# Performance work log

Hardware: AMD Instinct MI355X
Metric: run time of the kernel (lower is better)

The kernel has to match this reference:

```python
import jax, jax.numpy as jnp
import numpy as np

NX, NZ, NU, B = 16, 8, 4, 65536


def setup_inputs() -> dict:
    key = jax.random.key(0)
    ks = jax.random.split(key, 10)
    mu_prev = jax.random.normal(ks[0], (B, NX), dtype=jnp.float32)
    # PSD covariance per batch element: L L^T + 0.5 I
    L = 0.1 * jax.random.normal(ks[1], (B, NX, NX), dtype=jnp.float32)
    Sigma_prev = jnp.einsum('bij,bkj->bik', L, L) + 0.5 * jnp.eye(NX, dtype=jnp.float32)
    u = jax.random.normal(ks[2], (B, NU), dtype=jnp.float32)
    z = jax.random.normal(ks[3], (B, NZ), dtype=jnp.float32)
    # System matrices (shared across the batch); scaled to keep tanh unsaturated
    A = 0.1 * jax.random.normal(ks[4], (NX, NX), dtype=jnp.float32) + jnp.eye(NX, dtype=jnp.float32)
    Bm = 0.1 * jax.random.normal(ks[5], (NX, NU), dtype=jnp.float32)
    C = 0.2 * jax.random.normal(ks[6], (NZ, NX), dtype=jnp.float32)
    MQ = 0.1 * jax.random.normal(ks[7], (NZ, NZ), dtype=jnp.float32)
    Q = MQ @ MQ.T + 0.05 * jnp.eye(NZ, dtype=jnp.float32)   # measurement noise cov [nz,nz]
    MR = 0.1 * jax.random.normal(ks[8], (NX, NX), dtype=jnp.float32)
    R = MR @ MR.T + 0.01 * jnp.eye(NX, dtype=jnp.float32)   # process noise cov [nx,nx]
    return {'mu_prev': mu_prev, 'Sigma_prev': Sigma_prev, 'u': u, 'z': z,
            'A': A, 'Bm': Bm, 'C': C, 'Q': Q, 'R': R}


def reference(mu_prev, Sigma_prev, u, z, A, Bm, C, Q, R):
    # Discrete-time EKF propagate (already_discrete=True branch), batched via vmap.
    def f_sys(x, u):
        return jnp.tanh(A @ x + Bm @ u)

    def h_sys(x):
        return jnp.tanh(C @ x)

    I_nx = jnp.eye(NX, dtype=mu_prev.dtype)

    def step(mu, Sig, u_b, z_b):
        mu_bar = f_sys(mu, u_b)                      # [nx]
        G = jax.jacfwd(f_sys)(mu, u_b)               # [nx,nx] df/dx
        Sig_bar = R + G @ Sig @ G.T                  # [nx,nx]
        H = jax.jacfwd(h_sys)(mu_bar)                # [nz,nx] dh/dx
        tp = Sig_bar @ H.T                           # [nx,nz]
        K = tp @ jnp.linalg.inv(H @ tp + Q)          # [nx,nz] Kalman gain
        mu_now = mu_bar + K @ (z_b - h_sys(mu_bar))
        I_KH = I_nx - K @ H
        Sig_now = I_KH @ Sig_bar @ I_KH.T + K @ Q @ K.T  # Joseph form
        return mu_now, Sig_now

    return jax.vmap(step)(mu_prev, Sigma_prev, u, z)
```

## Files before the change

### kernel.cpp

```cpp
#include <hip/hip_runtime.h>
#include <math.h>


namespace {

constexpr int GROUPS = 16;
constexpr int TPB    = GROUPS * 16;

constexpr int O_VT  = 0;
constexpr int O_TPT = 0;
constexpr int O_SI  = 128;
constexpr int O_PIV = 192;
constexpr int O_VB  = 256;
constexpr int GS    = 312;

__device__ __forceinline__ float dot4(float4 a, float4 b) {
  return a.x*b.x + a.y*b.y + a.z*b.z + a.w*b.w;
}

__device__ __forceinline__ float tanh_fast(float x) {
  float e = __expf(2.0f * x);
  return 1.0f - 2.0f * __builtin_amdgcn_rcpf(e + 1.0f);
}

__global__ __launch_bounds__(TPB)
void ekf_kernel(const float* __restrict__ mu_prev,
                const float* __restrict__ Sig_prev,
                const float* __restrict__ U,
                const float* __restrict__ Z,
                const float* __restrict__ A,
                const float* __restrict__ Bm,
                const float* __restrict__ C,
                const float* __restrict__ Q,
                const float* __restrict__ R,
                float* __restrict__ mu_out,
                float* __restrict__ sig_out,
                int Btot)
{
  __shared__ float lds[GS * GROUPS];
  const int tid = threadIdx.x;
  const int g = tid >> 4;
  const int t = tid & 15;
  int e = blockIdx.x * GROUPS + g;
  if (e >= Btot) e = Btot - 1;
  float* L = lds + g * GS;

  float sig[16];
  {
    const float4* sp = (const float4*)(Sig_prev + (size_t)e * 256 + t * 16);
    #pragma unroll
    for (int c = 0; c < 4; c++) {
      float4 v = sp[c];
      sig[4*c+0] = v.x; sig[4*c+1] = v.y; sig[4*c+2] = v.z; sig[4*c+3] = v.w;
    }
  }

  float pre;
  {
    const float4* ar = (const float4*)(A + t * 16);
    const float4* mr = (const float4*)(mu_prev + (size_t)e * 16);
    pre = dot4(ar[0], mr[0]) + dot4(ar[1], mr[1])
        + dot4(ar[2], mr[2]) + dot4(ar[3], mr[3]);
    float4 b4 = *(const float4*)(Bm + t * 4);
    float4 u4 = *(const float4*)(U + (size_t)e * 4);
    pre += dot4(b4, u4);
  }
  const float mubar = tanh_fast(pre);
  const float dloc  = 1.0f - mubar * mubar;
  L[O_VB + t]      = mubar;
  L[O_VB + 16 + t] = dloc;
  __builtin_amdgcn_wave_barrier();

  if (t < 8) {
    const float4* cr = (const float4*)(C + t * 16);
    const float4* mb = (const float4*)(L + O_VB);
    float ph = dot4(cr[0], mb[0]) + dot4(cr[1], mb[1])
             + dot4(cr[2], mb[2]) + dot4(cr[3], mb[3]);
    float hb = tanh_fast(ph);
    L[O_VB + 32 + t] = hb;
    L[O_VB + 40 + t] = 1.0f - hb * hb;
  }
  __builtin_amdgcn_wave_barrier();

  float dh[8];
  {
    float4 d0 = *(const float4*)(L + O_VB + 40);
    float4 d1 = *(const float4*)(L + O_VB + 44);
    dh[0]=d0.x; dh[1]=d0.y; dh[2]=d0.z; dh[3]=d0.w;
    dh[4]=d1.x; dh[5]=d1.y; dh[6]=d1.z; dh[7]=d1.w;
  }

  #pragma unroll
  for (int j = 0; j < 16; j++) {
    float acc = 0.f;
    #pragma unroll
    for (int k = 0; k < 16; k++) acc += sig[k] * A[j*16 + k];
    L[O_VT + j*16 + t] = acc;
  }
  __builtin_amdgcn_wave_barrier();

  float sb[16];
  {
    float vcol[16];
    const float4* vt = (const float4*)(L + O_VT + t*16);
    #pragma unroll
    for (int c = 0; c < 4; c++) {
      float4 v = vt[c];
      vcol[4*c+0]=v.x; vcol[4*c+1]=v.y; vcol[4*c+2]=v.z; vcol[4*c+3]=v.w;
    }
    #pragma unroll
    for (int i = 0; i < 16; i++) {
      float acc = 0.f;
      #pragma unroll
      for (int k = 0; k < 16; k++) acc += A[i*16 + k] * vcol[k];
      sb[i] = acc;
    }
  }
  __builtin_amdgcn_wave_barrier();

  {
    const float4* rr = (const float4*)(R + t * 16);
    const float4* dv = (const float4*)(L + O_VB + 16);
    #pragma unroll
    for (int c = 0; c < 4; c++) {
      float4 r4 = rr[c];
      float4 d4 = dv[c];
      sb[4*c+0] = r4.x + dloc * sb[4*c+0] * d4.x;
      sb[4*c+1] = r4.y + dloc * sb[4*c+1] * d4.y;
      sb[4*c+2] = r4.z + dloc * sb[4*c+2] * d4.z;
      sb[4*c+3] = r4.w + dloc * sb[4*c+3] * d4.w;
    }
  }

  float tp[8];
  #pragma unroll
  for (int m = 0; m < 8; m++) {
    float acc = 0.f;
    #pragma unroll
    for (int k = 0; k < 16; k++) acc += sb[k] * C[m*16 + k];
    tp[m] = acc * dh[m];
    L[O_TPT + m*16 + t] = tp[m];
  }
  __builtin_amdgcn_wave_barrier();

  if (t < 8) {
    float tcol[16];
    const float4* tt = (const float4*)(L + O_TPT + t*16);
    #pragma unroll
    for (int c = 0; c < 4; c++) {
      float4 v = tt[c];
      tcol[4*c+0]=v.x; tcol[4*c+1]=v.y; tcol[4*c+2]=v.z; tcol[4*c+3]=v.w;
    }
    float s8[8];
    {
      float4 q0 = *(const float4*)(Q + t*8);
      float4 q1 = *(const float4*)(Q + t*8 + 4);
      float qv[8] = {q0.x,q0.y,q0.z,q0.w,q1.x,q1.y,q1.z,q1.w};
      #pragma unroll
      for (int m = 0; m < 8; m++) {
        float acc = 0.f;
        #pragma unroll
        for (int k = 0; k < 16; k++) acc += C[m*16 + k] * tcol[k];
        s8[m] = acc * dh[m] + qv[m];
      }
    }

    float x8[8];
    #pragma unroll
    for (int j = 0; j < 8; j++) x8[j] = (j == t) ? 1.0f : 0.0f;
    #pragma unroll
    for (int p = 0; p < 8; p++) {
      if (t == p) {
        float rcp = 1.0f / s8[p];
        #pragma unroll
        for (int j = 0; j < 8; j++) { s8[j] *= rcp; x8[j] *= rcp; }
        *((float4*)(L + O_PIV + 0))  = make_float4(s8[0], s8[1], s8[2], s8[3]);
        *((float4*)(L + O_PIV + 4))  = make_float4(s8[4], s8[5], s8[6], s8[7]);
        *((float4*)(L + O_PIV + 8))  = make_float4(x8[0], x8[1], x8[2], x8[3]);
        *((float4*)(L + O_PIV + 12)) = make_float4(x8[4], x8[5], x8[6], x8[7]);
      }
      __builtin_amdgcn_wave_barrier();
      if (t != p) {
        float f = s8[p];
        float4 pa = *(const float4*)(L + O_PIV + 0);
        float4 pb = *(const float4*)(L + O_PIV + 4);
        float4 pc = *(const float4*)(L + O_PIV + 8);
        float4 pd = *(const float4*)(L + O_PIV + 12);
        s8[0]-=f*pa.x; s8[1]-=f*pa.y; s8[2]-=f*pa.z; s8[3]-=f*pa.w;
        s8[4]-=f*pb.x; s8[5]-=f*pb.y; s8[6]-=f*pb.z; s8[7]-=f*pb.w;
        x8[0]-=f*pc.x; x8[1]-=f*pc.y; x8[2]-=f*pc.z; x8[3]-=f*pc.w;
        x8[4]-=f*pd.x; x8[5]-=f*pd.y; x8[6]-=f*pd.z; x8[7]-=f*pd.w;
      }
      __builtin_amdgcn_wave_barrier();
    }
    *((float4*)(L + O_SI + t*8 + 0)) = make_float4(x8[0], x8[1], x8[2], x8[3]);
    *((float4*)(L + O_SI + t*8 + 4)) = make_float4(x8[4], x8[5], x8[6], x8[7]);
  }
  __builtin_amdgcn_wave_barrier();

  float kreg[8] = {0,0,0,0,0,0,0,0};
  #pragma unroll
  for (int m = 0; m < 8; m++) {
    float tpm = tp[m];
    float4 a = *(const float4*)(L + O_SI + m*8 + 0);
    float4 b = *(const float4*)(L + O_SI + m*8 + 4);
    kreg[0]+=tpm*a.x; kreg[1]+=tpm*a.y; kreg[2]+=tpm*a.z; kreg[3]+=tpm*a.w;
    kreg[4]+=tpm*b.x; kreg[5]+=tpm*b.y; kreg[6]+=tpm*b.z; kreg[7]+=tpm*b.w;
  }

  {
    float4 z0 = *(const float4*)(Z + (size_t)e * 8);
    float4 z1 = *(const float4*)(Z + (size_t)e * 8 + 4);
    float4 h0 = *(const float4*)(L + O_VB + 32);
    float4 h1 = *(const float4*)(L + O_VB + 36);
    float mu_now = mubar
      + kreg[0]*(z0.x-h0.x) + kreg[1]*(z0.y-h0.y)
      + kreg[2]*(z0.z-h0.z) + kreg[3]*(z0.w-h0.w)
      + kreg[4]*(z1.x-h1.x) + kreg[5]*(z1.y-h1.y)
      + kreg[6]*(z1.z-h1.z) + kreg[7]*(z1.w-h1.w);
    mu_out[(size_t)e * 16 + t] = mu_now;
  }

  float out[16];
  #pragma unroll
  for (int i = 0; i < 16; i++) out[i] = sb[i];
  #pragma unroll
  for (int m = 0; m < 8; m++) {
    const float km = kreg[m];
    const float4* tr = (const float4*)(L + O_TPT + m*16);
    float4 t0 = tr[0], t1 = tr[1], t2 = tr[2], t3 = tr[3];
    out[0]  -= km*t0.x; out[1]  -= km*t0.y; out[2]  -= km*t0.z; out[3]  -= km*t0.w;
    out[4]  -= km*t1.x; out[5]  -= km*t1.y; out[6]  -= km*t1.z; out[7]  -= km*t1.w;
    out[8]  -= km*t2.x; out[9]  -= km*t2.y; out[10] -= km*t2.z; out[11] -= km*t2.w;
    out[12] -= km*t3.x; out[13] -= km*t3.y; out[14] -= km*t3.z; out[15] -= km*t3.w;
  }
  {
    float4* op = (float4*)(sig_out + (size_t)e * 256 + t * 16);
    op[0] = make_float4(out[0],  out[1],  out[2],  out[3]);
    op[1] = make_float4(out[4],  out[5],  out[6],  out[7]);
    op[2] = make_float4(out[8],  out[9],  out[10], out[11]);
    op[3] = make_float4(out[12], out[13], out[14], out[15]);
  }
}

}

extern "C" void kernel_launch(void* const* d_in, const int* in_sizes, int n_in,
                              void* d_out, int out_size, void* d_ws, size_t ws_size,
                              hipStream_t stream)
{
  const float* mu_prev = (const float*)d_in[0];
  const float* Sigma   = (const float*)d_in[1];
  const float* u       = (const float*)d_in[2];
  const float* z       = (const float*)d_in[3];
  const float* A       = (const float*)d_in[4];
  const float* Bm      = (const float*)d_in[5];
  const float* C       = (const float*)d_in[6];
  const float* Q       = (const float*)d_in[7];
  const float* R       = (const float*)d_in[8];

  const int Btot = in_sizes[0] / 16;
  float* mu_out  = (float*)d_out;
  float* sig_out = (float*)d_out + (size_t)Btot * 16;

  const int grid = (Btot + GROUPS - 1) / GROUPS;
  ekf_kernel<<<grid, TPB, 0, stream>>>(mu_prev, Sigma, u, z, A, Bm, C, Q, R,
                                       mu_out, sig_out, Btot);
}
```

Baseline: 164.9 us.

## Use 8 lanes per batch element and register-swizzle Gauss-Jordan inverse

Each batch element is now handled by 8 lanes instead of 16. Every lane owns two rows of the covariance, which halves the shared constant-matrix loads per FMA and keeps all 8 lanes busy in the innovation-covariance stage. The 8x8 Gauss-Jordan inversion now broadcasts pivot rows with ds_swizzle between lanes instead of LDS writes plus wave barriers. The cost is more registers per lane, which could reduce occupancy, and a more complex elimination step.

```diff
diff --git a/kernel.cpp b/kernel.cpp
--- a/kernel.cpp
+++ b/kernel.cpp
@@ -4,15 +4,18 @@
 
 namespace {
 
-constexpr int GROUPS = 16;
-constexpr int TPB    = GROUPS * 16;
+constexpr int LPE    = 8;
+constexpr int GROUPS = 32;
+constexpr int TPB    = GROUPS * LPE;
 
 constexpr int O_VT  = 0;
 constexpr int O_TPT = 0;
 constexpr int O_SI  = 128;
-constexpr int O_PIV = 192;
-constexpr int O_VB  = 256;
-constexpr int GS    = 312;
+constexpr int O_MU  = 256;
+constexpr int O_D   = 272;
+constexpr int O_H   = 288;
+constexpr int O_DH  = 296;
+constexpr int GS    = 308;
 
 __device__ __forceinline__ float dot4(float4 a, float4 b) {
   return a.x*b.x + a.y*b.y + a.z*b.z + a.w*b.w;
@@ -22,6 +25,26 @@
   float e = __expf(2.0f * x);
   return 1.0f - 2.0f * __builtin_amdgcn_rcpf(e + 1.0f);
 }
+
+#define SWZF(v, imm) __int_as_float(__builtin_amdgcn_ds_swizzle(__float_as_int(v), (imm)))
+
+#define GJ_STEP(P)                                                         \
+  {                                                                        \
+    float ps[8], px[8];                                                    \
+    _Pragma("unroll")                                                      \
+    for (int j = 0; j < 8; j++) {                                          \
+      if (j >= (P)) ps[j] = SWZF(s8[j], (((P) << 5) | 0x18));              \
+      else          px[j] = SWZF(x8[j], (((P) << 5) | 0x18));              \
+    }                                                                      \
+    const float rp = __builtin_amdgcn_rcpf(ps[(P)]);                       \
+    const float f  = (t == (P)) ? (ps[(P)] - 1.0f) : s8[(P)];              \
+    _Pragma("unroll")                                                      \
+    for (int j = 0; j < 8; j++) {                                          \
+      if (j > (P))      s8[j] -= f * (ps[j] * rp);                         \
+      else if (j < (P)) x8[j] -= f * (px[j] * rp);                         \
+    }                                                                      \
+    x8[(P)] -= f * rp;                                                     \
+  }
 
 __global__ __launch_bounds__(TPB)
 void ekf_kernel(const float* __restrict__ mu_prev,
@@ -39,207 +62,209 @@
 {
   __shared__ float lds[GS * GROUPS];
   const int tid = threadIdx.x;
-  const int g = tid >> 4;
-  const int t = tid & 15;
+  const int g = tid >> 3;
+  const int t = tid & 7;
   int e = blockIdx.x * GROUPS + g;
   if (e >= Btot) e = Btot - 1;
   float* L = lds + g * GS;
-
-  float sig[16];
-  {
-    const float4* sp = (const float4*)(Sig_prev + (size_t)e * 256 + t * 16);
+  const int r0 = t, r1 = t + 8;
+
+  float sig0[16], sig1[16];
+  {
+    const float4* s0 = (const float4*)(Sig_prev + (size_t)e * 256 + r0 * 16);
+    const float4* s1 = (const float4*)(Sig_prev + (size_t)e * 256 + r1 * 16);
     #pragma unroll
     for (int c = 0; c < 4; c++) {
-      float4 v = sp[c];
-      sig[4*c+0] = v.x; sig[4*c+1] = v.y; sig[4*c+2] = v.z; sig[4*c+3] = v.w;
-    }
-  }
-
-  float pre;
-  {
-    const float4* ar = (const float4*)(A + t * 16);
+      float4 v0 = s0[c], v1 = s1[c];
+      sig0[4*c+0]=v0.x; sig0[4*c+1]=v0.y; sig0[4*c+2]=v0.z; sig0[4*c+3]=v0.w;
+      sig1[4*c+0]=v1.x; sig1[4*c+1]=v1.y; sig1[4*c+2]=v1.z; sig1[4*c+3]=v1.w;
+    }
+  }
+
+  float mubar0, mubar1, d0loc, d1loc;
+  {
     const float4* mr = (const float4*)(mu_prev + (size_t)e * 16);
-    pre = dot4(ar[0], mr[0]) + dot4(ar[1], mr[1])
-        + dot4(ar[2], mr[2]) + dot4(ar[3], mr[3]);
-    float4 b4 = *(const float4*)(Bm + t * 4);
+    float4 m0 = mr[0], m1 = mr[1], m2 = mr[2], m3 = mr[3];
+    const float4* a0 = (const float4*)(A + r0 * 16);
+    const float4* a1 = (const float4*)(A + r1 * 16);
+    float p0 = dot4(a0[0],m0)+dot4(a0[1],m1)+dot4(a0[2],m2)+dot4(a0[3],m3);
+    float p1 = dot4(a1[0],m0)+dot4(a1[1],m1)+dot4(a1[2],m2)+dot4(a1[3],m3);
     float4 u4 = *(const float4*)(U + (size_t)e * 4);
-    pre += dot4(b4, u4);
-  }
-  const float mubar = tanh_fast(pre);
-  const float dloc  = 1.0f - mubar * mubar;
-  L[O_VB + t]      = mubar;
-  L[O_VB + 16 + t] = dloc;
-  __builtin_amdgcn_wave_barrier();
-
-  if (t < 8) {
+    p0 += dot4(*(const float4*)(Bm + r0 * 4), u4);
+    p1 += dot4(*(const float4*)(Bm + r1 * 4), u4);
+    mubar0 = tanh_fast(p0); d0loc = 1.0f - mubar0 * mubar0;
+    mubar1 = tanh_fast(p1); d1loc = 1.0f - mubar1 * mubar1;
+  }
+  L[O_MU + r0] = mubar0; L[O_MU + r1] = mubar1;
+  L[O_D  + r0] = d0loc;  L[O_D  + r1] = d1loc;
+  __builtin_amdgcn_wave_barrier();
+
+  float4 ct0, ct1, ct2, ct3;
+  float dhl;
+  {
     const float4* cr = (const float4*)(C + t * 16);
-    const float4* mb = (const float4*)(L + O_VB);
-    float ph = dot4(cr[0], mb[0]) + dot4(cr[1], mb[1])
-             + dot4(cr[2], mb[2]) + dot4(cr[3], mb[3]);
-    float hb = tanh_fast(ph);
-    L[O_VB + 32 + t] = hb;
-    L[O_VB + 40 + t] = 1.0f - hb * hb;
-  }
-  __builtin_amdgcn_wave_barrier();
-
+    ct0 = cr[0]; ct1 = cr[1]; ct2 = cr[2]; ct3 = cr[3];
+    const float4* mb = (const float4*)(L + O_MU);
+    float ph = dot4(ct0,mb[0])+dot4(ct1,mb[1])+dot4(ct2,mb[2])+dot4(ct3,mb[3]);
+    float hb = tanh_fast(ph); dhl = 1.0f - hb * hb;
+    L[O_H + t] = hb; L[O_DH + t] = dhl;
+  }
+  __builtin_amdgcn_wave_barrier();
   float dh[8];
   {
-    float4 d0 = *(const float4*)(L + O_VB + 40);
-    float4 d1 = *(const float4*)(L + O_VB + 44);
-    dh[0]=d0.x; dh[1]=d0.y; dh[2]=d0.z; dh[3]=d0.w;
-    dh[4]=d1.x; dh[5]=d1.y; dh[6]=d1.z; dh[7]=d1.w;
+    float4 v0 = *(const float4*)(L + O_DH);
+    float4 v1 = *(const float4*)(L + O_DH + 4);
+    dh[0]=v0.x; dh[1]=v0.y; dh[2]=v0.z; dh[3]=v0.w;
+    dh[4]=v1.x; dh[5]=v1.y; dh[6]=v1.z; dh[7]=v1.w;
   }
 
   #pragma unroll
   for (int j = 0; j < 16; j++) {
-    float acc = 0.f;
-    #pragma unroll
-    for (int k = 0; k < 16; k++) acc += sig[k] * A[j*16 + k];
-    L[O_VT + j*16 + t] = acc;
-  }
-  __builtin_amdgcn_wave_barrier();
-
-  float sb[16];
-  {
-    float vcol[16];
-    const float4* vt = (const float4*)(L + O_VT + t*16);
+    float acc0 = 0.f, acc1 = 0.f;
+    #pragma unroll
+    for (int k = 0; k < 16; k++) {
+      float a = A[j*16 + k];
+      acc0 += sig0[k] * a; acc1 += sig1[k] * a;
+    }
+    L[O_VT + j*16 + r0] = acc0;
+    L[O_VT + j*16 + r1] = acc1;
+  }
+  __builtin_amdgcn_wave_barrier();
+
+  float sb0[16], sb1[16];
+  {
+    float v0[16], v1[16];
+    const float4* p0 = (const float4*)(L + O_VT + r0 * 16);
+    const float4* p1 = (const float4*)(L + O_VT + r1 * 16);
     #pragma unroll
     for (int c = 0; c < 4; c++) {
-      float4 v = vt[c];
-      vcol[4*c+0]=v.x; vcol[4*c+1]=v.y; vcol[4*c+2]=v.z; vcol[4*c+3]=v.w;
+      float4 x0 = p0[c], x1 = p1[c];
+      v0[4*c+0]=x0.x; v0[4*c+1]=x0.y; v0[4*c+2]=x0.z; v0[4*c+3]=x0.w;
+      v1[4*c+0]=x1.x; v1[4*c+1]=x1.y; v1[4*c+2]=x1.z; v1[4*c+3]=x1.w;
     }
     #pragma unroll
     for (int i = 0; i < 16; i++) {
-      float acc = 0.f;
+      float acc0 = 0.f, acc1 = 0.f;
       #pragma unroll
-      for (int k = 0; k < 16; k++) acc += A[i*16 + k] * vcol[k];
-      sb[i] = acc;
-    }
-  }
-  __builtin_amdgcn_wave_barrier();
-
-  {
-    const float4* rr = (const float4*)(R + t * 16);
-    const float4* dv = (const float4*)(L + O_VB + 16);
+      for (int k = 0; k < 16; k++) {
+        float a = A[i*16 + k];
+        acc0 += a * v0[k]; acc1 += a * v1[k];
+      }
+      sb0[i] = acc0; sb1[i] = acc1;
+    }
+  }
+  __builtin_amdgcn_wave_barrier();
+
+  {
+    const float4* rr0 = (const float4*)(R + r0 * 16);
+    const float4* rr1 = (const float4*)(R + r1 * 16);
+    const float4* dv  = (const float4*)(L + O_D);
     #pragma unroll
     for (int c = 0; c < 4; c++) {
-      float4 r4 = rr[c];
-      float4 d4 = dv[c];
-      sb[4*c+0] = r4.x + dloc * sb[4*c+0] * d4.x;
-      sb[4*c+1] = r4.y + dloc * sb[4*c+1] * d4.y;
-      sb[4*c+2] = r4.z + dloc * sb[4*c+2] * d4.z;
-      sb[4*c+3] = r4.w + dloc * sb[4*c+3] * d4.w;
-    }
-  }
-
-  float tp[8];
+      float4 ra = rr0[c], rb = rr1[c], dd = dv[c];
+      sb0[4*c+0] = ra.x + d0loc*sb0[4*c+0]*dd.x;
+      sb0[4*c+1] = ra.y + d0loc*sb0[4*c+1]*dd.y;
+      sb0[4*c+2] = ra.z + d0loc*sb0[4*c+2]*dd.z;
+      sb0[4*c+3] = ra.w + d0loc*sb0[4*c+3]*dd.w;
+      sb1[4*c+0] = rb.x + d1loc*sb1[4*c+0]*dd.x;
+      sb1[4*c+1] = rb.y + d1loc*sb1[4*c+1]*dd.y;
+      sb1[4*c+2] = rb.z + d1loc*sb1[4*c+2]*dd.z;
+      sb1[4*c+3] = rb.w + d1loc*sb1[4*c+3]*dd.w;
+    }
+  }
+
+  float tp0[8], tp1[8];
   #pragma unroll
   for (int m = 0; m < 8; m++) {
-    float acc = 0.f;
-    #pragma unroll
-    for (int k = 0; k < 16; k++) acc += sb[k] * C[m*16 + k];
-    tp[m] = acc * dh[m];
-    L[O_TPT + m*16 + t] = tp[m];
-  }
-  __builtin_amdgcn_wave_barrier();
-
-  if (t < 8) {
-    float tcol[16];
-    const float4* tt = (const float4*)(L + O_TPT + t*16);
-    #pragma unroll
-    for (int c = 0; c < 4; c++) {
-      float4 v = tt[c];
-      tcol[4*c+0]=v.x; tcol[4*c+1]=v.y; tcol[4*c+2]=v.z; tcol[4*c+3]=v.w;
-    }
-    float s8[8];
-    {
-      float4 q0 = *(const float4*)(Q + t*8);
-      float4 q1 = *(const float4*)(Q + t*8 + 4);
-      float qv[8] = {q0.x,q0.y,q0.z,q0.w,q1.x,q1.y,q1.z,q1.w};
-      #pragma unroll
-      for (int m = 0; m < 8; m++) {
-        float acc = 0.f;
-        #pragma unroll
-        for (int k = 0; k < 16; k++) acc += C[m*16 + k] * tcol[k];
-        s8[m] = acc * dh[m] + qv[m];
-      }
-    }
-
-    float x8[8];
-    #pragma unroll
-    for (int j = 0; j < 8; j++) x8[j] = (j == t) ? 1.0f : 0.0f;
-    #pragma unroll
-    for (int p = 0; p < 8; p++) {
-      if (t == p) {
-        float rcp = 1.0f / s8[p];
-        #pragma unroll
-        for (int j = 0; j < 8; j++) { s8[j] *= rcp; x8[j] *= rcp; }
-        *((float4*)(L + O_PIV + 0))  = make_float4(s8[0], s8[1], s8[2], s8[3]);
-        *((float4*)(L + O_PIV + 4))  = make_float4(s8[4], s8[5], s8[6], s8[7]);
-        *((float4*)(L + O_PIV + 8))  = make_float4(x8[0], x8[1], x8[2], x8[3]);
-        *((float4*)(L + O_PIV + 12)) = make_float4(x8[4], x8[5], x8[6], x8[7]);
-      }
-      __builtin_amdgcn_wave_barrier();
-      if (t != p) {
-        float f = s8[p];
-        float4 pa = *(const float4*)(L + O_PIV + 0);
-        float4 pb = *(const float4*)(L + O_PIV + 4);
-        float4 pc = *(const float4*)(L + O_PIV + 8);
-        float4 pd = *(const float4*)(L + O_PIV + 12);
-        s8[0]-=f*pa.x; s8[1]-=f*pa.y; s8[2]-=f*pa.z; s8[3]-=f*pa.w;
-        s8[4]-=f*pb.x; s8[5]-=f*pb.y; s8[6]-=f*pb.z; s8[7]-=f*pb.w;
-        x8[0]-=f*pc.x; x8[1]-=f*pc.y; x8[2]-=f*pc.z; x8[3]-=f*pc.w;
-        x8[4]-=f*pd.x; x8[5]-=f*pd.y; x8[6]-=f*pd.z; x8[7]-=f*pd.w;
-      }
-      __builtin_amdgcn_wave_barrier();
-    }
-    *((float4*)(L + O_SI + t*8 + 0)) = make_float4(x8[0], x8[1], x8[2], x8[3]);
-    *((float4*)(L + O_SI + t*8 + 4)) = make_float4(x8[4], x8[5], x8[6], x8[7]);
-  }
-  __builtin_amdgcn_wave_barrier();
-
-  float kreg[8] = {0,0,0,0,0,0,0,0};
+    float acc0 = 0.f, acc1 = 0.f;
+    #pragma unroll
+    for (int k = 0; k < 16; k++) {
+      float c = C[m*16 + k];
+      acc0 += sb0[k] * c; acc1 += sb1[k] * c;
+    }
+    tp0[m] = acc0 * dh[m]; tp1[m] = acc1 * dh[m];
+    L[O_TPT + m*16 + r0] = tp0[m];
+    L[O_TPT + m*16 + r1] = tp1[m];
+  }
+  __builtin_amdgcn_wave_barrier();
+
+  float s8[8];
+  {
+    float4 q0 = *(const float4*)(Q + t * 8);
+    float4 q1 = *(const float4*)(Q + t * 8 + 4);
+    float qv[8] = {q0.x,q0.y,q0.z,q0.w,q1.x,q1.y,q1.z,q1.w};
+    #pragma unroll
+    for (int m = 0; m < 8; m++) {
+      const float4* tr = (const float4*)(L + O_TPT + m * 16);
+      float acc = dot4(ct0,tr[0]) + dot4(ct1,tr[1])
+                + dot4(ct2,tr[2]) + dot4(ct3,tr[3]);
+      s8[m] = acc * dhl + qv[m];
+    }
+  }
+
+  float x8[8];
+  #pragma unroll
+  for (int j = 0; j < 8; j++) x8[j] = (j == t) ? 1.0f : 0.0f;
+  GJ_STEP(0) GJ_STEP(1) GJ_STEP(2) GJ_STEP(3)
+  GJ_STEP(4) GJ_STEP(5) GJ_STEP(6) GJ_STEP(7)
+
+  *((float4*)(L + O_SI + t*8 + 0)) = make_float4(x8[0], x8[1], x8[2], x8[3]);
+  *((float4*)(L + O_SI + t*8 + 4)) = make_float4(x8[4], x8[5], x8[6], x8[7]);
+  __builtin_amdgcn_wave_barrier();
+
+  float k0[8] = {0,0,0,0,0,0,0,0};
+  float k1[8] = {0,0,0,0,0,0,0,0};
   #pragma unroll
   for (int m = 0; m < 8; m++) {
-    float tpm = tp[m];
     float4 a = *(const float4*)(L + O_SI + m*8 + 0);
     float4 b = *(const float4*)(L + O_SI + m*8 + 4);
-    kreg[0]+=tpm*a.x; kreg[1]+=tpm*a.y; kreg[2]+=tpm*a.z; kreg[3]+=tpm*a.w;
-    kreg[4]+=tpm*b.x; kreg[5]+=tpm*b.y; kreg[6]+=tpm*b.z; kreg[7]+=tpm*b.w;
+    float f0 = tp0[m], f1 = tp1[m];
+    k0[0]+=f0*a.x; k0[1]+=f0*a.y; k0[2]+=f0*a.z; k0[3]+=f0*a.w;
+    k0[4]+=f0*b.x; k0[5]+=f0*b.y; k0[6]+=f0*b.z; k0[7]+=f0*b.w;
+    k1[0]+=f1*a.x; k1[1]+=f1*a.y; k1[2]+=f1*a.z; k1[3]+=f1*a.w;
+    k1[4]+=f1*b.x; k1[5]+=f1*b.y; k1[6]+=f1*b.z; k1[7]+=f1*b.w;
   }
 
   {
     float4 z0 = *(const float4*)(Z + (size_t)e * 8);
     float4 z1 = *(const float4*)(Z + (size_t)e * 8 + 4);
-    float4 h0 = *(const float4*)(L + O_VB + 32);
-    float4 h1 = *(const float4*)(L + O_VB + 36);
-    float mu_now = mubar
-      + kreg[0]*(z0.x-h0.x) + kreg[1]*(z0.y-h0.y)
-      + kreg[2]*(z0.z-h0.z) + kreg[3]*(z0.w-h0.w)
-      + kreg[4]*(z1.x-h1.x) + kreg[5]*(z1.y-h1.y)
-      + kreg[6]*(z1.z-h1.z) + kreg[7]*(z1.w-h1.w);
-    mu_out[(size_t)e * 16 + t] = mu_now;
-  }
-
-  float out[16];
-  #pragma unroll
-  for (int i = 0; i < 16; i++) out[i] = sb[i];
+    float4 h0 = *(const float4*)(L + O_H);
+    float4 h1 = *(const float4*)(L + O_H + 4);
+    float i0=z0.x-h0.x, i1=z0.y-h0.y, i2=z0.z-h0.z, i3=z0.w-h0.w;
+    float i4=z1.x-h1.x, i5=z1.y-h1.y, i6=z1.z-h1.z, i7=z1.w-h1.w;
+    float mu0 = mubar0 + k0[0]*i0+k0[1]*i1+k0[2]*i2+k0[3]*i3
+                       + k0[4]*i4+k0[5]*i5+k0[6]*i6+k0[7]*i7;
+    float mu1 = mubar1 + k1[0]*i0+k1[1]*i1+k1[2]*i2+k1[3]*i3
+                       + k1[4]*i4+k1[5]*i5+k1[6]*i6+k1[7]*i7;
+    mu_out[(size_t)e * 16 + r0] = mu0;
+    mu_out[(size_t)e * 16 + r1] = mu1;
+  }
+
   #pragma unroll
   for (int m = 0; m < 8; m++) {
-    const float km = kreg[m];
-    const float4* tr = (const float4*)(L + O_TPT + m*16);
+    const float4* tr = (const float4*)(L + O_TPT + m * 16);
     float4 t0 = tr[0], t1 = tr[1], t2 = tr[2], t3 = tr[3];
-    out[0]  -= km*t0.x; out[1]  -= km*t0.y; out[2]  -= km*t0.z; out[3]  -= km*t0.w;
-    out[4]  -= km*t1.x; out[5]  -= km*t1.y; out[6]  -= km*t1.z; out[7]  -= km*t1.w;
-    out[8]  -= km*t2.x; out[9]  -= km*t2.y; out[10] -= km*t2.z; out[11] -= km*t2.w;
-    out[12] -= km*t3.x; out[13] -= km*t3.y; out[14] -= km*t3.z; out[15] -= km*t3.w;
-  }
-  {
-    float4* op = (float4*)(sig_out + (size_t)e * 256 + t * 16);
-    op[0] = make_float4(out[0],  out[1],  out[2],  out[3]);
-    op[1] = make_float4(out[4],  out[5],  out[6],  out[7]);
-    op[2] = make_float4(out[8],  out[9],  out[10], out[11]);
-    op[3] = make_float4(out[12], out[13], out[14], out[15]);
+    float km0 = k0[m], km1 = k1[m];
+    sb0[0] -=km0*t0.x; sb0[1] -=km0*t0.y; sb0[2] -=km0*t0.z; sb0[3] -=km0*t0.w;
+    sb0[4] -=km0*t1.x; sb0[5] -=km0*t1.y; sb0[6] -=km0*t1.z; sb0[7] -=km0*t1.w;
+    sb0[8] -=km0*t2.x; sb0[9] -=km0*t2.y; sb0[10]-=km0*t2.z; sb0[11]-=km0*t2.w;
+    sb0[12]-=km0*t3.x; sb0[13]-=km0*t3.y; sb0[14]-=km0*t3.z; sb0[15]-=km0*t3.w;
+    sb1[0] -=km1*t0.x; sb1[1] -=km1*t0.y; sb1[2] -=km1*t0.z; sb1[3] -=km1*t0.w;
+    sb1[4] -=km1*t1.x; sb1[5] -=km1*t1.y; sb1[6] -=km1*t1.z; sb1[7] -=km1*t1.w;
+    sb1[8] -=km1*t2.x; sb1[9] -=km1*t2.y; sb1[10]-=km1*t2.z; sb1[11]-=km1*t2.w;
+    sb1[12]-=km1*t3.x; sb1[13]-=km1*t3.y; sb1[14]-=km1*t3.z; sb1[15]-=km1*t3.w;
+  }
+  {
+    float4* o0 = (float4*)(sig_out + (size_t)e * 256 + r0 * 16);
+    float4* o1 = (float4*)(sig_out + (size_t)e * 256 + r1 * 16);
+    o0[0] = make_float4(sb0[0],  sb0[1],  sb0[2],  sb0[3]);
+    o0[1] = make_float4(sb0[4],  sb0[5],  sb0[6],  sb0[7]);
+    o0[2] = make_float4(sb0[8],  sb0[9],  sb0[10], sb0[11]);
+    o0[3] = make_float4(sb0[12], sb0[13], sb0[14], sb0[15]);
+    o1[0] = make_float4(sb1[0],  sb1[1],  sb1[2],  sb1[3]);
+    o1[1] = make_float4(sb1[4],  sb1[5],  sb1[6],  sb1[7]);
+    o1[2] = make_float4(sb1[8],  sb1[9],  sb1[10], sb1[11]);
+    o1[3] = make_float4(sb1[12], sb1[13], sb1[14], sb1[15]);
   }
 }
 
```

Result: faster. 159.7 us (-3.2%).

## Replace LDS-broadcast Gauss-Jordan inversion with ds_swizzle register exchange

Applied to the files above, without the earlier changes.

The 8x8 innovation-covariance inversion no longer broadcasts pivot rows through LDS with two wave barriers per pivot. Each lane now pulls the pivot row from lane P of its 8-lane subgroup with ds_swizzle and divides using the hardware rcp instead of a full-precision divide. The S-matrix build is duplicated across both 8-lane halves so the whole 16-lane group runs the solve without divergence. The change also batches LDS stores after the register computations and folds the R/Jacobian scaling into the Sigma_bar matmul, at the cost of extra registers and slightly lower reciprocal precision.

```diff
diff --git a/kernel.cpp b/kernel.cpp
--- a/kernel.cpp
+++ b/kernel.cpp
@@ -6,13 +6,15 @@
 
 constexpr int GROUPS = 16;
 constexpr int TPB    = GROUPS * 16;
+constexpr int GS     = 424;
 
 constexpr int O_VT  = 0;
 constexpr int O_TPT = 0;
 constexpr int O_SI  = 128;
-constexpr int O_PIV = 192;
-constexpr int O_VB  = 256;
-constexpr int GS    = 312;
+constexpr int O_MU  = 256;
+constexpr int O_D   = 272;
+constexpr int O_H   = 288;
+constexpr int O_DH  = 296;
 
 __device__ __forceinline__ float dot4(float4 a, float4 b) {
   return a.x*b.x + a.y*b.y + a.z*b.z + a.w*b.w;
@@ -22,6 +24,26 @@
   float e = __expf(2.0f * x);
   return 1.0f - 2.0f * __builtin_amdgcn_rcpf(e + 1.0f);
 }
+
+#define SWZF(v, imm) __int_as_float(__builtin_amdgcn_ds_swizzle(__float_as_int(v), (imm)))
+
+#define GJ_STEP(P)                                                         \
+  {                                                                        \
+    float ps[8], px[8];                                                    \
+    _Pragma("unroll")                                                      \
+    for (int j = 0; j < 8; j++) {                                          \
+      if (j >= (P)) ps[j] = SWZF(s8[j], (((P) << 5) | 0x18));              \
+      else          px[j] = SWZF(x8[j], (((P) << 5) | 0x18));              \
+    }                                                                      \
+    const float rp = __builtin_amdgcn_rcpf(ps[(P)]);                       \
+    const float f  = (tl == (P)) ? (ps[(P)] - 1.0f) : s8[(P)];             \
+    _Pragma("unroll")                                                      \
+    for (int j = 0; j < 8; j++) {                                          \
+      if (j > (P))      s8[j] -= f * (ps[j] * rp);                         \
+      else if (j < (P)) x8[j] -= f * (px[j] * rp);                         \
+    }                                                                      \
+    x8[(P)] -= f * rp;                                                     \
+  }
 
 __global__ __launch_bounds__(TPB)
 void ekf_kernel(const float* __restrict__ mu_prev,
@@ -39,8 +61,9 @@
 {
   __shared__ float lds[GS * GROUPS];
   const int tid = threadIdx.x;
-  const int g = tid >> 4;
-  const int t = tid & 15;
+  const int g  = tid >> 4;
+  const int t  = tid & 15;
+  const int tl = t & 7;
   int e = blockIdx.x * GROUPS + g;
   if (e >= Btot) e = Btot - 1;
   float* L = lds + g * GS;
@@ -55,144 +78,123 @@
     }
   }
 
-  float pre;
+  float mubar, dloc;
   {
     const float4* ar = (const float4*)(A + t * 16);
     const float4* mr = (const float4*)(mu_prev + (size_t)e * 16);
-    pre = dot4(ar[0], mr[0]) + dot4(ar[1], mr[1])
-        + dot4(ar[2], mr[2]) + dot4(ar[3], mr[3]);
+    float pre = dot4(ar[0], mr[0]) + dot4(ar[1], mr[1])
+              + dot4(ar[2], mr[2]) + dot4(ar[3], mr[3]);
     float4 b4 = *(const float4*)(Bm + t * 4);
     float4 u4 = *(const float4*)(U + (size_t)e * 4);
     pre += dot4(b4, u4);
-  }
-  const float mubar = tanh_fast(pre);
-  const float dloc  = 1.0f - mubar * mubar;
-  L[O_VB + t]      = mubar;
-  L[O_VB + 16 + t] = dloc;
+    mubar = tanh_fast(pre);
+    dloc  = 1.0f - mubar * mubar;
+  }
+  L[O_MU + t] = mubar;
+  L[O_D  + t] = dloc;
   __builtin_amdgcn_wave_barrier();
 
   if (t < 8) {
     const float4* cr = (const float4*)(C + t * 16);
-    const float4* mb = (const float4*)(L + O_VB);
+    const float4* mb = (const float4*)(L + O_MU);
     float ph = dot4(cr[0], mb[0]) + dot4(cr[1], mb[1])
              + dot4(cr[2], mb[2]) + dot4(cr[3], mb[3]);
     float hb = tanh_fast(ph);
-    L[O_VB + 32 + t] = hb;
-    L[O_VB + 40 + t] = 1.0f - hb * hb;
+    L[O_H  + t] = hb;
+    L[O_DH + t] = 1.0f - hb * hb;
   }
   __builtin_amdgcn_wave_barrier();
 
   float dh[8];
   {
-    float4 d0 = *(const float4*)(L + O_VB + 40);
-    float4 d1 = *(const float4*)(L + O_VB + 44);
+    float4 d0 = *(const float4*)(L + O_DH);
+    float4 d1 = *(const float4*)(L + O_DH + 4);
     dh[0]=d0.x; dh[1]=d0.y; dh[2]=d0.z; dh[3]=d0.w;
     dh[4]=d1.x; dh[5]=d1.y; dh[6]=d1.z; dh[7]=d1.w;
   }
 
+  float vv[16];
   #pragma unroll
   for (int j = 0; j < 16; j++) {
     float acc = 0.f;
     #pragma unroll
     for (int k = 0; k < 16; k++) acc += sig[k] * A[j*16 + k];
-    L[O_VT + j*16 + t] = acc;
-  }
-  __builtin_amdgcn_wave_barrier();
-
-  float sb[16];
-  {
-    float vcol[16];
-    const float4* vt = (const float4*)(L + O_VT + t*16);
+    vv[j] = acc;
+  }
+  #pragma unroll
+  for (int j = 0; j < 16; j++) L[O_VT + j*16 + t] = vv[j];
+  __builtin_amdgcn_wave_barrier();
+
+  float vcol[16];
+  {
+    const float4* vt = (const float4*)(L + O_VT + t * 16);
     #pragma unroll
     for (int c = 0; c < 4; c++) {
       float4 v = vt[c];
       vcol[4*c+0]=v.x; vcol[4*c+1]=v.y; vcol[4*c+2]=v.z; vcol[4*c+3]=v.w;
+    }
+  }
+
+  float sb[16];
+  {
+    float rr[16], dv[16];
+    const float4* rp4 = (const float4*)(R + t * 16);
+    const float4* dp4 = (const float4*)(L + O_D);
+    #pragma unroll
+    for (int c = 0; c < 4; c++) {
+      float4 r4 = rp4[c], d4 = dp4[c];
+      rr[4*c+0]=r4.x; rr[4*c+1]=r4.y; rr[4*c+2]=r4.z; rr[4*c+3]=r4.w;
+      dv[4*c+0]=d4.x; dv[4*c+1]=d4.y; dv[4*c+2]=d4.z; dv[4*c+3]=d4.w;
     }
     #pragma unroll
     for (int i = 0; i < 16; i++) {
       float acc = 0.f;
       #pragma unroll
       for (int k = 0; k < 16; k++) acc += A[i*16 + k] * vcol[k];
-      sb[i] = acc;
-    }
-  }
-  __builtin_amdgcn_wave_barrier();
-
-  {
-    const float4* rr = (const float4*)(R + t * 16);
-    const float4* dv = (const float4*)(L + O_VB + 16);
-    #pragma unroll
-    for (int c = 0; c < 4; c++) {
-      float4 r4 = rr[c];
-      float4 d4 = dv[c];
-      sb[4*c+0] = r4.x + dloc * sb[4*c+0] * d4.x;
-      sb[4*c+1] = r4.y + dloc * sb[4*c+1] * d4.y;
-      sb[4*c+2] = r4.z + dloc * sb[4*c+2] * d4.z;
-      sb[4*c+3] = r4.w + dloc * sb[4*c+3] * d4.w;
-    }
-  }
-
-  float tp[8];
+      sb[i] = rr[i] + dloc * acc * dv[i];
+    }
+  }
+
+  float tpv[8];
   #pragma unroll
   for (int m = 0; m < 8; m++) {
     float acc = 0.f;
     #pragma unroll
     for (int k = 0; k < 16; k++) acc += sb[k] * C[m*16 + k];
-    tp[m] = acc * dh[m];
-    L[O_TPT + m*16 + t] = tp[m];
-  }
-  __builtin_amdgcn_wave_barrier();
+    tpv[m] = acc * dh[m];
+  }
+  #pragma unroll
+  for (int m = 0; m < 8; m++) L[O_TPT + m*16 + t] = tpv[m];
+  __builtin_amdgcn_wave_barrier();
+
+  float s8[8];
+  {
+    float tc[16];
+    const float4* tt = (const float4*)(L + O_TPT + tl * 16);
+    #pragma unroll
+    for (int c = 0; c < 4; c++) {
+      float4 v = tt[c];
+      tc[4*c+0]=v.x; tc[4*c+1]=v.y; tc[4*c+2]=v.z; tc[4*c+3]=v.w;
+    }
+    float4 q0 = *(const float4*)(Q + tl * 8);
+    float4 q1 = *(const float4*)(Q + tl * 8 + 4);
+    float qv[8] = {q0.x,q0.y,q0.z,q0.w,q1.x,q1.y,q1.z,q1.w};
+    #pragma unroll
+    for (int m = 0; m < 8; m++) {
+      float acc = 0.f;
+      #pragma unroll
+      for (int k = 0; k < 16; k++) acc += C[m*16 + k] * tc[k];
+      s8[m] = acc * dh[m] + qv[m];
+    }
+  }
+
+  float x8[8];
+  #pragma unroll
+  for (int j = 0; j < 8; j++) x8[j] = (j == tl) ? 1.0f : 0.0f;
+  GJ_STEP(0) GJ_STEP(1) GJ_STEP(2) GJ_STEP(3)
+  GJ_STEP(4) GJ_STEP(5) GJ_STEP(6) GJ_STEP(7)
 
   if (t < 8) {
-    float tcol[16];
-    const float4* tt = (const float4*)(L + O_TPT + t*16);
-    #pragma unroll
-    for (int c = 0; c < 4; c++) {
-      float4 v = tt[c];
-      tcol[4*c+0]=v.x; tcol[4*c+1]=v.y; tcol[4*c+2]=v.z; tcol[4*c+3]=v.w;
-    }
-    float s8[8];
-    {
-      float4 q0 = *(const float4*)(Q + t*8);
-      float4 q1 = *(const float4*)(Q + t*8 + 4);
-      float qv[8] = {q0.x,q0.y,q0.z,q0.w,q1.x,q1.y,q1.z,q1.w};
-      #pragma unroll
-      for (int m = 0; m < 8; m++) {
-        float acc = 0.f;
-        #pragma unroll
-        for (int k = 0; k < 16; k++) acc += C[m*16 + k] * tcol[k];
-        s8[m] = acc * dh[m] + qv[m];
-      }
-    }
-
-    float x8[8];
-    #pragma unroll
-    for (int j = 0; j < 8; j++) x8[j] = (j == t) ? 1.0f : 0.0f;
-    #pragma unroll
-    for (int p = 0; p < 8; p++) {
-      if (t == p) {
-        float rcp = 1.0f / s8[p];
-        #pragma unroll
-        for (int j = 0; j < 8; j++) { s8[j] *= rcp; x8[j] *= rcp; }
-        *((float4*)(L + O_PIV + 0))  = make_float4(s8[0], s8[1], s8[2], s8[3]);
-        *((float4*)(L + O_PIV + 4))  = make_float4(s8[4], s8[5], s8[6], s8[7]);
-        *((float4*)(L + O_PIV + 8))  = make_float4(x8[0], x8[1], x8[2], x8[3]);
-        *((float4*)(L + O_PIV + 12)) = make_float4(x8[4], x8[5], x8[6], x8[7]);
-      }
-      __builtin_amdgcn_wave_barrier();
-      if (t != p) {
-        float f = s8[p];
-        float4 pa = *(const float4*)(L + O_PIV + 0);
-        float4 pb = *(const float4*)(L + O_PIV + 4);
-        float4 pc = *(const float4*)(L + O_PIV + 8);
-        float4 pd = *(const float4*)(L + O_PIV + 12);
-        s8[0]-=f*pa.x; s8[1]-=f*pa.y; s8[2]-=f*pa.z; s8[3]-=f*pa.w;
-        s8[4]-=f*pb.x; s8[5]-=f*pb.y; s8[6]-=f*pb.z; s8[7]-=f*pb.w;
-        x8[0]-=f*pc.x; x8[1]-=f*pc.y; x8[2]-=f*pc.z; x8[3]-=f*pc.w;
-        x8[4]-=f*pd.x; x8[5]-=f*pd.y; x8[6]-=f*pd.z; x8[7]-=f*pd.w;
-      }
-      __builtin_amdgcn_wave_barrier();
-    }
     *((float4*)(L + O_SI + t*8 + 0)) = make_float4(x8[0], x8[1], x8[2], x8[3]);
     *((float4*)(L + O_SI + t*8 + 4)) = make_float4(x8[4], x8[5], x8[6], x8[7]);
   }
@@ -201,18 +203,18 @@
   float kreg[8] = {0,0,0,0,0,0,0,0};
   #pragma unroll
   for (int m = 0; m < 8; m++) {
-    float tpm = tp[m];
     float4 a = *(const float4*)(L + O_SI + m*8 + 0);
     float4 b = *(const float4*)(L + O_SI + m*8 + 4);
-    kreg[0]+=tpm*a.x; kreg[1]+=tpm*a.y; kreg[2]+=tpm*a.z; kreg[3]+=tpm*a.w;
-    kreg[4]+=tpm*b.x; kreg[5]+=tpm*b.y; kreg[6]+=tpm*b.z; kreg[7]+=tpm*b.w;
+    float f = tpv[m];
+    kreg[0]+=f*a.x; kreg[1]+=f*a.y; kreg[2]+=f*a.z; kreg[3]+=f*a.w;
+    kreg[4]+=f*b.x; kreg[5]+=f*b.y; kreg[6]+=f*b.z; kreg[7]+=f*b.w;
   }
 
   {
     float4 z0 = *(const float4*)(Z + (size_t)e * 8);
     float4 z1 = *(const float4*)(Z + (size_t)e * 8 + 4);
-    float4 h0 = *(const float4*)(L + O_VB + 32);
-    float4 h1 = *(const float4*)(L + O_VB + 36);
+    float4 h0 = *(const float4*)(L + O_H);
+    float4 h1 = *(const float4*)(L + O_H + 4);
     float mu_now = mubar
       + kreg[0]*(z0.x-h0.x) + kreg[1]*(z0.y-h0.y)
       + kreg[2]*(z0.z-h0.z) + kreg[3]*(z0.w-h0.w)
@@ -226,9 +228,9 @@
   for (int i = 0; i < 16; i++) out[i] = sb[i];
   #pragma unroll
   for (int m = 0; m < 8; m++) {
-    const float km = kreg[m];
-    const float4* tr = (const float4*)(L + O_TPT + m*16);
+    const float4* tr = (const float4*)(L + O_TPT + m * 16);
     float4 t0 = tr[0], t1 = tr[1], t2 = tr[2], t3 = tr[3];
+    float km = kreg[m];
     out[0]  -= km*t0.x; out[1]  -= km*t0.y; out[2]  -= km*t0.z; out[3]  -= km*t0.w;
     out[4]  -= km*t1.x; out[5]  -= km*t1.y; out[6]  -= km*t1.z; out[7]  -= km*t1.w;
     out[8]  -= km*t2.x; out[9]  -= km*t2.y; out[10] -= km*t2.z; out[11] -= km*t2.w;
```

After: 160.7 us. 1.03x faster.
